# Kernel tuning notes

Hardware: AMD Instinct MI355X
Metric: run time of the kernel (lower is better)

The kernel has to match this reference:

```python
import jax, jax.numpy as jnp
import numpy as np

H = 400          # hidden_layers
D_CUR = 3 + 2 + 50   # X_CUR + X_WIN + X_ET
D_AC = 3 + 49        # X_AC + X_T
D_AP = 6 + 49        # X_AP + X_T


def _cell(x, h1, c1, h2, c2, Wx, U, b):
    """2-child child-sum LSTM cell (inferred CustomLSTMCell).
    x: [T, in]; h*/c*: [T, H]; Wx: [in, 4H]; U: [H, 4H]; b: [4H].
    Gate order: i, f, o, u. f uses a per-child recurrent term.
    """
    g = x @ Wx + b                            # [T, 4H]
    gi, gf, go, gu = jnp.split(g, 4, axis=-1)
    Ui, Uf, Uo, Uu = jnp.split(U, 4, axis=-1)
    hs = h1 + h2
    i = jax.nn.sigmoid(gi + hs @ Ui)
    f1 = jax.nn.sigmoid(gf + h1 @ Uf)
    f2 = jax.nn.sigmoid(gf + h2 @ Uf)
    o = jax.nn.sigmoid(go + hs @ Uo)
    u = jnp.tanh(gu + hs @ Uu)
    c = i * u + f1 * c1 + f2 * c2
    return o * jnp.tanh(c), c


def setup_inputs() -> dict:
    key = jax.random.key(0)
    T, IN = 8192, 55
    ks = iter(jax.random.split(key, 40))

    def p(*shape):
        return jax.random.normal(next(ks), shape, dtype=jnp.float32) * 0.05

    inp = {
        "x_temp": jax.random.normal(next(ks), (T, IN), dtype=jnp.float32),
        "x_air": jax.random.normal(next(ks), (T, IN), dtype=jnp.float32),
    }
    for name, d_in in [("t1", IN), ("t2", H), ("t3", H), ("a1", IN), ("a2", H), ("a3", H)]:
        inp[f"Wx_{name}"] = p(d_in, 4 * H)
        inp[f"U_{name}"] = p(H, 4 * H)
        inp[f"b_{name}"] = p(4 * H)
    inp["W_cur"] = p(2 * H, D_CUR); inp["b_cur"] = p(D_CUR)
    inp["W_ac"] = p(H, D_AC);       inp["b_ac"] = p(D_AC)
    inp["W_ap"] = p(H, D_AP);       inp["b_ap"] = p(D_AP)
    return inp


def reference(x_temp, x_air,
              Wx_t1, U_t1, b_t1, Wx_t2, U_t2, b_t2, Wx_t3, U_t3, b_t3,
              Wx_a1, U_a1, b_a1, Wx_a2, U_a2, b_a2, Wx_a3, U_a3, b_a3,
              W_cur, b_cur, W_ac, b_ac, W_ap, b_ap):
    T = x_temp.shape[0]
    z = jnp.zeros((T, H), dtype=x_temp.dtype)
    # States are re-zeroed every timestep in the original loop, so all
    # timesteps are independent and we batch them along axis 0.
    ht, ct = _cell(x_temp, z, z, z, z, Wx_t1, U_t1, b_t1)
    ha, ca = _cell(x_air,  z, z, z, z, Wx_a1, U_a1, b_a1)
    ht2, ct2 = _cell(ht, ht, ct, ha, ca, Wx_t2, U_t2, b_t2)
    ha2, ca2 = _cell(ha, ht, ct, ha, ca, Wx_a2, U_a2, b_a2)
    ht3, _ = _cell(ht2, ht2, ct2, ha2, ca2, Wx_t3, U_t3, b_t3)
    ha3, _ = _cell(ha2, ht2, ct2, ha2, ca2, Wx_a3, U_a3, b_a3)
    out_cur_win_t = jnp.concatenate([ht3, ha3], axis=-1) @ W_cur + b_cur  # [T, 55]
    out_ac_tet = ht3 @ W_ac + b_ac                                        # [T, 52]
    out_ap_aet = ha3 @ W_ap + b_ap                                        # [T, 55]
    return out_cur_win_t, out_ac_tet, out_ap_aet
```

## Files before the change

### kernel.cpp

```cpp
#include <hip/hip_runtime.h>
#include <hip/hip_bf16.h>

typedef unsigned short u16;
typedef unsigned int u32;
typedef unsigned long long u64;
typedef __attribute__((ext_vector_type(4))) float f32x4;
typedef __attribute__((ext_vector_type(8))) short s16x8;

__device__ inline u16 f2bf(float f) {
  union { float f; u32 u; } v; v.f = f;
  u32 r = (v.u + 0x7FFFu + ((v.u >> 16) & 1u)) >> 16;
  return (u16)r;
}
__device__ inline float bf2f(u16 h) { return __uint_as_float((u32)h << 16); }
__device__ inline float sigf(float x) { return 1.0f / (1.0f + __expf(-x)); }
__device__ inline float tanhf_(float x) {
  float ax = fabsf(x);
  float e = __expf(-2.0f * ax);
  float r = (1.0f - e) / (1.0f + e);
  return copysignf(r, x);
}
__device__ inline f32x4 ld4bf(const u16* p) {
  u64 v = *(const u64*)p;
  f32x4 r;
  r.x = __uint_as_float((u32)(v & 0xFFFFu) << 16);
  r.y = __uint_as_float((u32)((v >> 16) & 0xFFFFu) << 16);
  r.z = __uint_as_float((u32)((v >> 32) & 0xFFFFu) << 16);
  r.w = __uint_as_float((u32)((v >> 48) & 0xFFFFu) << 16);
  return r;
}
__device__ inline void gload16(const u16* g, u16* l) {
  __builtin_amdgcn_global_load_lds(
      (const __attribute__((address_space(1))) void*)(g),
      (__attribute__((address_space(3))) void*)(l), 16, 0, 0);
}

#define GLD 4096

__global__ void zero_pads(u16* __restrict__ A1, u16* __restrict__ A2,
                          u16* __restrict__ A3) {
  int idx = blockIdx.x * 256 + threadIdx.x;
  if (idx >= 196608) return;
  int b = idx / 65536, r = idx % 65536;
  int t = r / 8, q = r % 8;
  u16* A = (b == 0) ? A1 : (b == 1) ? A2 : A3;
  *(u64*)(A + (size_t)t * 832 + 800 + q * 4) = 0ULL;
}

__global__ void pad_cast(const float* __restrict__ src, u16* __restrict__ dst,
                         int srcCols, int dstCols, int rows) {
  int idx = blockIdx.x * 256 + threadIdx.x;
  if (idx >= rows * dstCols) return;
  int r = idx / dstCols, c = idx % dstCols;
  float v = (c < srcCols) ? src[r * srcCols + c] : 0.f;
  dst[idx] = f2bf(v);
}

__global__ void transpose_cast(const float* __restrict__ src, u16* __restrict__ dst,
                               int srcK, int srcN) {
  int idx = blockIdx.x * 256 + threadIdx.x;
  if (idx >= 64 * 1664) return;
  int k = idx / 1664, n = idx % 1664;
  float v = (k < srcK && n < srcN) ? src[k * srcN + n] : 0.f;
  dst[n * 64 + k] = f2bf(v);
}

__global__ void build_cell_B(const float* __restrict__ WxT, const float* __restrict__ UT,
                             const float* __restrict__ WxA, const float* __restrict__ UA,
                             u16* __restrict__ dst) {
  int idx = blockIdx.x * 256 + threadIdx.x;
  if (idx >= 4096 * 832) return;
  int r = idx / 4096, np = idx % 4096;
  int cell = np >> 11;
  int n = np & 2047;
  float v = 0.f;
  if (n < 2000 && r < 800) {
    int g = n / 400, j = n % 400;
    bool htside = (r < 400);
    int rr = htside ? r : r - 400;
    const float* Wx = cell ? WxA : WxT;
    const float* U  = cell ? UA  : UT;
    int gc = (g == 0) ? j : (g <= 2) ? 400 + j : (g == 3) ? 800 + j : 1200 + j;
    float wx = Wx[rr * 1600 + gc];
    float uu = U [rr * 1600 + gc];
    if (cell == 0) {
      if (htside) v = (g == 2) ? wx : wx + uu;
      else        v = (g == 1) ? 0.f : uu;
    } else {
      if (htside) v = (g == 2) ? 0.f : uu;
      else        v = (g == 1) ? wx : wx + uu;
    }
  }
  dst[(size_t)np * 832 + r] = f2bf(v);
}

__global__ void build_proj_B(const float* __restrict__ Wcur, const float* __restrict__ Wac,
                             const float* __restrict__ Wap, u16* __restrict__ dst) {
  int idx = blockIdx.x * 256 + threadIdx.x;
  if (idx >= 256 * 832) return;
  int n = idx / 832, r = idx % 832;
  float v = 0.f;
  if (r < 800) {
    if (n < 55) v = Wcur[r * 55 + n];
    else if (n < 107) { if (r < 400) v = Wac[r * 52 + (n - 55)]; }
    else if (n < 162) { if (r >= 400) v = Wap[(r - 400) * 55 + (n - 107)]; }
  }
  dst[idx] = f2bf(v);
}

__global__ __launch_bounds__(256) void gemm_lds(
    const u16* __restrict__ A, const u16* __restrict__ Bt,
    u16* __restrict__ C, int K, int ldc) {
  __shared__ u16 As[128 * 64];
  __shared__ u16 Bs[128 * 64];
  const int tid = threadIdx.x;
  const int lane = tid & 63;
  const int wid = tid >> 6;

  const int nwg = gridDim.x * gridDim.y;
  const int bid = blockIdx.y * gridDim.x + blockIdx.x;
  const int swz = (bid & 7) * (nwg >> 3) + (bid >> 3);
  const int m0 = (swz / gridDim.x) * 128;
  const int n0 = (swz % gridDim.x) * 128;

  const int wm = (wid >> 1) << 6;
  const int wn = (wid & 1) << 6;

  f32x4 acc[4][4];
#pragma unroll
  for (int i = 0; i < 4; ++i)
#pragma unroll
    for (int j = 0; j < 4; ++j) acc[i][j] = (f32x4){0.f, 0.f, 0.f, 0.f};

  const int nkt = K >> 6;
  const int l8 = lane >> 3, lb = lane & 7;
  const int scol = (lb ^ l8) << 3;
  const u16* gA = A + (size_t)(m0 + wid * 8 + l8) * K + scol;
  const u16* gB = Bt + (size_t)(n0 + wid * 8 + l8) * K + scol;
  u16* lA = As + wid * 8 * 64;
  u16* lB = Bs + wid * 8 * 64;

  const int kq = (lane >> 4) << 3;
  const int rrow = lane & 15;

  for (int kt = 0; kt < nkt; ++kt) {
    __syncthreads();
    const u16* pa = gA + kt * 64;
    const u16* pb = gB + kt * 64;
#pragma unroll
    for (int c = 0; c < 4; ++c) {
      gload16(pa + (size_t)(c * 32) * K, lA + c * 2048);
      gload16(pb + (size_t)(c * 32) * K, lB + c * 2048);
    }
    __syncthreads();
#pragma unroll
    for (int half = 0; half < 2; ++half) {
      const int kk = half * 32 + kq;
      s16x8 af[4], bfr[4];
#pragma unroll
      for (int f = 0; f < 4; ++f) {
        int ar = wm + f * 16 + rrow;
        af[f] = *(const s16x8*)((const char*)As + ar * 128 + ((kk * 2) ^ ((ar & 7) << 4)));
        int br = wn + f * 16 + rrow;
        bfr[f] = *(const s16x8*)((const char*)Bs + br * 128 + ((kk * 2) ^ ((br & 7) << 4)));
      }
#pragma unroll
      for (int i = 0; i < 4; ++i)
#pragma unroll
        for (int j = 0; j < 4; ++j)
          acc[i][j] = __builtin_amdgcn_mfma_f32_16x16x32_bf16(af[i], bfr[j], acc[i][j], 0, 0, 0);
    }
  }

  const int crow0 = m0 + wm + ((lane >> 4) << 2);
  const int ccol0 = n0 + wn + rrow;
#pragma unroll
  for (int i = 0; i < 4; ++i)
#pragma unroll
    for (int j = 0; j < 4; ++j)
#pragma unroll
      for (int r = 0; r < 4; ++r)
        C[(size_t)(crow0 + i * 16 + r) * ldc + (ccol0 + j * 16)] = f2bf(acc[i][j][r]);
}

__global__ void ep1(const u16* __restrict__ G,
                    const float* __restrict__ bT, const float* __restrict__ bA,
                    u16* __restrict__ Aout,
                    float* __restrict__ CT, float* __restrict__ CA) {
  int idx = blockIdx.x * 256 + threadIdx.x;
  if (idx >= 8192 * 200) return;
  int t = idx / 200, r = idx % 200;
  int cell = r / 100, j0 = (r % 100) * 4;
  const u16* g = G + (size_t)t * GLD + cell * 2048;
  const float* b = cell ? bA : bT;
  float* Cout = cell ? CA : CT;
  f32x4 ip = ld4bf(g + j0);
  f32x4 op = ld4bf(g + 800 + j0);
  f32x4 up = ld4bf(g + 1200 + j0);
  u64 hv = 0;
  f32x4 cv;
#pragma unroll
  for (int k = 0; k < 4; ++k) {
    int j = j0 + k;
    float c = sigf(ip[k] + b[j]) * tanhf_(up[k] + b[1200 + j]);
    float h = sigf(op[k] + b[800 + j]) * tanhf_(c);
    cv[k] = c;
    hv |= (u64)f2bf(h) << (16 * k);
  }
  *(u64*)(Aout + (size_t)t * 832 + cell * 400 + j0) = hv;
  *(f32x4*)(Cout + (size_t)t * 400 + j0) = cv;
}

__global__ void ep2(const u16* __restrict__ G,
                    const float* __restrict__ bT, const float* __restrict__ bA,
                    const float* __restrict__ C1, const float* __restrict__ C2,
                    u16* __restrict__ Aout,
                    float* __restrict__ CT, float* __restrict__ CA) {
  int idx = blockIdx.x * 256 + threadIdx.x;
  if (idx >= 8192 * 200) return;
  int t = idx / 200, r = idx % 200;
  int cell = r / 100, j0 = (r % 100) * 4;
  const u16* g = G + (size_t)t * GLD + cell * 2048;
  const float* b = cell ? bA : bT;
  float* Cout = cell ? CA : CT;
  f32x4 ip  = ld4bf(g + j0);
  f32x4 f1p = ld4bf(g + 400 + j0);
  f32x4 f2p = ld4bf(g + 800 + j0);
  f32x4 op  = ld4bf(g + 1200 + j0);
  f32x4 up  = ld4bf(g + 1600 + j0);
  f32x4 c1 = *(const f32x4*)(C1 + (size_t)t * 400 + j0);
  f32x4 c2 = *(const f32x4*)(C2 + (size_t)t * 400 + j0);
  u64 hv = 0;
  f32x4 cv;
#pragma unroll
  for (int k = 0; k < 4; ++k) {
    int j = j0 + k;
    float c = sigf(ip[k] + b[j]) * tanhf_(up[k] + b[1200 + j])
            + sigf(f1p[k] + b[400 + j]) * c1[k]
            + sigf(f2p[k] + b[400 + j]) * c2[k];
    float h = sigf(op[k] + b[800 + j]) * tanhf_(c);
    cv[k] = c;
    hv |= (u64)f2bf(h) << (16 * k);
  }
  *(u64*)(Aout + (size_t)t * 832 + cell * 400 + j0) = hv;
  if (Cout) *(f32x4*)(Cout + (size_t)t * 400 + j0) = cv;
}

__global__ void ep_out(const u16* __restrict__ G,
                       const float* __restrict__ bcur, const float* __restrict__ bac,
                       const float* __restrict__ bap, float* __restrict__ out) {
  int idx = blockIdx.x * 256 + threadIdx.x;
  if (idx >= 8192 * 162) return;
  int t = idx / 162, j = idx % 162;
  float v = bf2f(G[(size_t)t * GLD + j]);
  if (j < 55)       out[t * 55 + j] = v + bcur[j];
  else if (j < 107) out[450560 + t * 52 + (j - 55)] = v + bac[j - 55];
  else              out[876544 + t * 55 + (j - 107)] = v + bap[j - 107];
}

extern "C" void kernel_launch(void* const* d_in, const int* in_sizes, int n_in,
                              void* d_out, int out_size, void* d_ws, size_t ws_size,
                              hipStream_t stream) {
  const float* x_temp = (const float*)d_in[0];
  const float* x_air  = (const float*)d_in[1];
  const float* Wx_t1  = (const float*)d_in[2];
  const float* b_t1   = (const float*)d_in[4];
  const float* Wx_t2  = (const float*)d_in[5];
  const float* U_t2   = (const float*)d_in[6];
  const float* b_t2   = (const float*)d_in[7];
  const float* Wx_t3  = (const float*)d_in[8];
  const float* U_t3   = (const float*)d_in[9];
  const float* b_t3   = (const float*)d_in[10];
  const float* Wx_a1  = (const float*)d_in[11];
  const float* b_a1   = (const float*)d_in[13];
  const float* Wx_a2  = (const float*)d_in[14];
  const float* U_a2   = (const float*)d_in[15];
  const float* b_a2   = (const float*)d_in[16];
  const float* Wx_a3  = (const float*)d_in[17];
  const float* U_a3   = (const float*)d_in[18];
  const float* b_a3   = (const float*)d_in[19];
  const float* W_cur  = (const float*)d_in[20];
  const float* b_cur  = (const float*)d_in[21];
  const float* W_ac   = (const float*)d_in[22];
  const float* b_ac   = (const float*)d_in[23];
  const float* W_ap   = (const float*)d_in[24];
  const float* b_ap   = (const float*)d_in[25];

  char* ws = (char*)d_ws;
  u16*   A0t = (u16*)(ws + 0);
  u16*   A0a = (u16*)(ws + 1048576);
  u16*   B1t = (u16*)(ws + 2097152);
  u16*   B1a = (u16*)(ws + 2310144);
  u16*   Bp  = (u16*)(ws + 2523136);
  u16*   A1  = (u16*)(ws + 2949120);
  u16*   A2  = (u16*)(ws + 16580608);
  u16*   A3  = (u16*)(ws + 30212096);
  float* Ct  = (float*)(ws + 43843584);
  float* Ca  = (float*)(ws + 56950784);
  float* C2t = (float*)(ws + 70057984);
  float* C2a = (float*)(ws + 83165184);
  u16*   B2  = (u16*)(ws + 96272384);
  u16*   B3  = (u16*)(ws + 103088128);
  u16*   G   = (u16*)(ws + 109903872);
  float* out = (float*)d_out;

  dim3 blk(256);
  zero_pads<<<768, blk, 0, stream>>>(A1, A2, A3);
  pad_cast<<<2048, blk, 0, stream>>>(x_temp, A0t, 55, 64, 8192);
  pad_cast<<<2048, blk, 0, stream>>>(x_air,  A0a, 55, 64, 8192);
  transpose_cast<<<416, blk, 0, stream>>>(Wx_t1, B1t, 55, 1600);
  transpose_cast<<<416, blk, 0, stream>>>(Wx_a1, B1a, 55, 1600);
  build_cell_B<<<13312, blk, 0, stream>>>(Wx_t2, U_t2, Wx_a2, U_a2, B2);
  build_cell_B<<<13312, blk, 0, stream>>>(Wx_t3, U_t3, Wx_a3, U_a3, B3);
  build_proj_B<<<832, blk, 0, stream>>>(W_cur, W_ac, W_ap, Bp);

  gemm_lds<<<dim3(13, 64), blk, 0, stream>>>(A0t, B1t, G, 64, GLD);
  gemm_lds<<<dim3(13, 64), blk, 0, stream>>>(A0a, B1a, G + 2048, 64, GLD);
  ep1<<<6400, blk, 0, stream>>>(G, b_t1, b_a1, A1, Ct, Ca);
  gemm_lds<<<dim3(32, 64), blk, 0, stream>>>(A1, B2, G, 832, GLD);
  ep2<<<6400, blk, 0, stream>>>(G, b_t2, b_a2, Ct, Ca, A2, C2t, C2a);
  gemm_lds<<<dim3(32, 64), blk, 0, stream>>>(A2, B3, G, 832, GLD);
  ep2<<<6400, blk, 0, stream>>>(G, b_t3, b_a3, C2t, C2a, A3, nullptr, nullptr);
  gemm_lds<<<dim3(2, 64), blk, 0, stream>>>(A3, Bp, G, 832, GLD);
  ep_out<<<5184, blk, 0, stream>>>(G, b_cur, b_ac, b_ap, out);
}
```

Baseline: 417.7 us.

## Add triple-buffered pipelined GEMM for layer-2/3 cells and tile-transpose weight build

Adds a new 512-thread GEMM kernel for the two large 8192x4096x832 cell GEMMs. It uses 256x128 tiles, a triple-buffered LDS pipeline fed by async global-to-LDS loads with explicit vmcnt waits, an XOR-swizzled LDS layout and workgroup-ID swizzling. This is meant to hide global load latency and avoid bank conflicts. The weight-building kernel is also rewritten to go through a shared-memory tile transpose, so its global reads and writes are coalesced instead of strided. The new GEMM uses 144KB of LDS and hardcoded sizes, which limits occupancy and flexibility.

```diff
diff --git a/kernel.cpp b/kernel.cpp
--- a/kernel.cpp
+++ b/kernel.cpp
@@ -65,33 +65,50 @@
   dst[n * 64 + k] = f2bf(v);
 }
 
-__global__ void build_cell_B(const float* __restrict__ WxT, const float* __restrict__ UT,
-                             const float* __restrict__ WxA, const float* __restrict__ UA,
-                             u16* __restrict__ dst) {
-  int idx = blockIdx.x * 256 + threadIdx.x;
-  if (idx >= 4096 * 832) return;
-  int r = idx / 4096, np = idx % 4096;
-  int cell = np >> 11;
-  int n = np & 2047;
-  float v = 0.f;
-  if (n < 2000 && r < 800) {
-    int g = n / 400, j = n % 400;
-    bool htside = (r < 400);
-    int rr = htside ? r : r - 400;
-    const float* Wx = cell ? WxA : WxT;
-    const float* U  = cell ? UA  : UT;
-    int gc = (g == 0) ? j : (g <= 2) ? 400 + j : (g == 3) ? 800 + j : 1200 + j;
-    float wx = Wx[rr * 1600 + gc];
-    float uu = U [rr * 1600 + gc];
-    if (cell == 0) {
-      if (htside) v = (g == 2) ? wx : wx + uu;
-      else        v = (g == 1) ? 0.f : uu;
-    } else {
-      if (htside) v = (g == 2) ? 0.f : uu;
-      else        v = (g == 1) ? wx : wx + uu;
-    }
-  }
-  dst[(size_t)np * 832 + r] = f2bf(v);
+__global__ __launch_bounds__(256) void build_cell_B(
+    const float* __restrict__ WxT, const float* __restrict__ UT,
+    const float* __restrict__ WxA, const float* __restrict__ UA,
+    u16* __restrict__ dst) {
+  __shared__ float tile[64][65];
+  const int np0 = blockIdx.x * 64;
+  const int r0 = blockIdx.y * 64;
+  const int tx = threadIdx.x & 63, ty = threadIdx.x >> 6;
+
+  const int np = np0 + tx;
+  const int cell = np >> 11;
+  const int n = np & 2047;
+  const float* Wx = cell ? WxA : WxT;
+  const float* U  = cell ? UA  : UT;
+  int g = 0, j = 0, gc = 0;
+  if (n < 2000) {
+    g = n / 400; j = n % 400;
+    gc = (g == 0) ? j : (g <= 2) ? 400 + j : (g == 3) ? 800 + j : 1200 + j;
+  }
+#pragma unroll
+  for (int it = 0; it < 16; ++it) {
+    int r = r0 + it * 4 + ty;
+    float v = 0.f;
+    if (n < 2000 && r < 800) {
+      bool htside = (r < 400);
+      int rr = htside ? r : r - 400;
+      float wx = Wx[rr * 1600 + gc];
+      float uu = U [rr * 1600 + gc];
+      if (cell == 0) {
+        if (htside) v = (g == 2) ? wx : wx + uu;
+        else        v = (g == 1) ? 0.f : uu;
+      } else {
+        if (htside) v = (g == 2) ? 0.f : uu;
+        else        v = (g == 1) ? wx : wx + uu;
+      }
+    }
+    tile[tx][it * 4 + ty] = v;
+  }
+  __syncthreads();
+#pragma unroll
+  for (int it = 0; it < 16; ++it) {
+    int npw = np0 + it * 4 + ty;
+    dst[(size_t)npw * 832 + r0 + tx] = f2bf(tile[it * 4 + ty][tx]);
+  }
 }
 
 __global__ void build_proj_B(const float* __restrict__ Wcur, const float* __restrict__ Wac,
@@ -181,6 +198,123 @@
 #pragma unroll
       for (int r = 0; r < 4; ++r)
         C[(size_t)(crow0 + i * 16 + r) * ldc + (ccol0 + j * 16)] = f2bf(acc[i][j][r]);
+}
+
+#define PK 832
+#define PNKT 13
+#define ABY 32768
+#define BBY 16384
+#define BUFB 49152
+
+__global__ __launch_bounds__(512, 2) void gemm_pipe(
+    const u16* __restrict__ A, const u16* __restrict__ Bt,
+    u16* __restrict__ C, int ldc) {
+  __shared__ char sm[3 * BUFB];
+  const int tid = threadIdx.x;
+  const int lane = tid & 63;
+  const int wid = tid >> 6;
+
+  const int nwg = gridDim.x * gridDim.y;
+  const int bid = blockIdx.y * gridDim.x + blockIdx.x;
+  const int swz = (bid & 7) * (nwg >> 3) + (bid >> 3);
+  const int m0 = (swz / gridDim.x) * 256;
+  const int n0 = (swz % gridDim.x) * 128;
+
+  const int wr = wid >> 1;
+  const int wc = wid & 1;
+
+  f32x4 acc[4][4];
+#pragma unroll
+  for (int i = 0; i < 4; ++i)
+#pragma unroll
+    for (int j = 0; j < 4; ++j) acc[i][j] = (f32x4){0.f, 0.f, 0.f, 0.f};
+
+  const int q = lane >> 3, lb = lane & 7;
+  const int scol = (lb ^ q) << 3;
+  const u16* gA = A + (size_t)(m0 + wid * 8 + q) * PK + scol;
+  const u16* gB = Bt + (size_t)(n0 + wid * 8 + q) * PK + scol;
+  const int wrow = wid * 8;
+
+  const int kq = (lane >> 4) << 3;
+  const int rrow = lane & 15;
+
+#define STAGE(kt, buf)                                                        \
+  {                                                                           \
+    char* bb = sm + (buf) * BUFB;                                             \
+    const u16* pa = gA + (kt) * 64;                                           \
+    const u16* pb = gB + (kt) * 64;                                           \
+    gload16(pa,                  (u16*)(bb + (0 * 64 + wrow) * 128));         \
+    gload16(pa + 64 * PK,        (u16*)(bb + (1 * 64 + wrow) * 128));         \
+    gload16(pa + 128 * PK,       (u16*)(bb + (2 * 64 + wrow) * 128));         \
+    gload16(pa + 192 * PK,       (u16*)(bb + (3 * 64 + wrow) * 128));         \
+    gload16(pb,                  (u16*)(bb + ABY + (0 * 64 + wrow) * 128));   \
+    gload16(pb + 64 * PK,        (u16*)(bb + ABY + (1 * 64 + wrow) * 128));   \
+  }
+
+  STAGE(0, 0);
+  STAGE(1, 1);
+
+  int cbuf = 0;
+  int sbuf = 2;
+  for (int k = 0; k < PNKT; ++k) {
+    __builtin_amdgcn_sched_barrier(0);
+    __builtin_amdgcn_s_barrier();
+    if (k < PNKT - 2) {
+      STAGE(k + 2, sbuf);
+      asm volatile("s_waitcnt vmcnt(12)" ::: "memory");
+    } else if (k == PNKT - 2) {
+      asm volatile("s_waitcnt vmcnt(6)" ::: "memory");
+    } else {
+      asm volatile("s_waitcnt vmcnt(0)" ::: "memory");
+    }
+    __builtin_amdgcn_s_barrier();
+    __builtin_amdgcn_sched_barrier(0);
+
+    const char* bb = sm + cbuf * BUFB;
+    s16x8 af[4][2], bfr[4][2];
+#pragma unroll
+    for (int i = 0; i < 4; ++i) {
+      int ar = wr * 64 + i * 16 + rrow;
+      const char* base = bb + ar * 128;
+#pragma unroll
+      for (int h = 0; h < 2; ++h) {
+        int kk2 = (h * 32 + kq) * 2;
+        af[i][h] = *(const s16x8*)(base + (kk2 ^ ((ar & 7) << 4)));
+      }
+    }
+#pragma unroll
+    for (int jf = 0; jf < 4; ++jf) {
+      int br = wc * 64 + jf * 16 + rrow;
+      const char* base = bb + ABY + br * 128;
+#pragma unroll
+      for (int h = 0; h < 2; ++h) {
+        int kk2 = (h * 32 + kq) * 2;
+        bfr[jf][h] = *(const s16x8*)(base + (kk2 ^ ((br & 7) << 4)));
+      }
+    }
+#pragma unroll
+    for (int i = 0; i < 4; ++i)
+#pragma unroll
+      for (int jf = 0; jf < 4; ++jf)
+#pragma unroll
+        for (int h = 0; h < 2; ++h)
+          acc[i][jf] = __builtin_amdgcn_mfma_f32_16x16x32_bf16(
+              af[i][h], bfr[jf][h], acc[i][jf], 0, 0, 0);
+
+    cbuf = (cbuf == 2) ? 0 : cbuf + 1;
+    sbuf = (sbuf == 2) ? 0 : sbuf + 1;
+  }
+#undef STAGE
+
+  const int crow0 = m0 + wr * 64 + ((lane >> 4) << 2);
+  const int ccol0 = n0 + wc * 64 + rrow;
+#pragma unroll
+  for (int i = 0; i < 4; ++i)
+#pragma unroll
+    for (int jf = 0; jf < 4; ++jf)
+#pragma unroll
+      for (int r = 0; r < 4; ++r)
+        C[(size_t)(crow0 + i * 16 + r) * ldc + (ccol0 + jf * 16)] = f2bf(acc[i][jf][r]);
 }
 
 __global__ void ep1(const u16* __restrict__ G,
@@ -310,16 +444,16 @@
   pad_cast<<<2048, blk, 0, stream>>>(x_air,  A0a, 55, 64, 8192);
   transpose_cast<<<416, blk, 0, stream>>>(Wx_t1, B1t, 55, 1600);
   transpose_cast<<<416, blk, 0, stream>>>(Wx_a1, B1a, 55, 1600);
-  build_cell_B<<<13312, blk, 0, stream>>>(Wx_t2, U_t2, Wx_a2, U_a2, B2);
-  build_cell_B<<<13312, blk, 0, stream>>>(Wx_t3, U_t3, Wx_a3, U_a3, B3);
+  build_cell_B<<<dim3(64, 13), blk, 0, stream>>>(Wx_t2, U_t2, Wx_a2, U_a2, B2);
+  build_cell_B<<<dim3(64, 13), blk, 0, stream>>>(Wx_t3, U_t3, Wx_a3, U_a3, B3);
   build_proj_B<<<832, blk, 0, stream>>>(W_cur, W_ac, W_ap, Bp);
 
   gemm_lds<<<dim3(13, 64), blk, 0, stream>>>(A0t, B1t, G, 64, GLD);
   gemm_lds<<<dim3(13, 64), blk, 0, stream>>>(A0a, B1a, G + 2048, 64, GLD);
   ep1<<<6400, blk, 0, stream>>>(G, b_t1, b_a1, A1, Ct, Ca);
-  gemm_lds<<<dim3(32, 64), blk, 0, stream>>>(A1, B2, G, 832, GLD);
+  gemm_pipe<<<dim3(32, 32), dim3(512), 0, stream>>>(A1, B2, G, GLD);
   ep2<<<6400, blk, 0, stream>>>(G, b_t2, b_a2, Ct, Ca, A2, C2t, C2a);
-  gemm_lds<<<dim3(32, 64), blk, 0, stream>>>(A2, B3, G, 832, GLD);
+  gemm_pipe<<<dim3(32, 32), dim3(512), 0, stream>>>(A2, B3, G, GLD);
   ep2<<<6400, blk, 0, stream>>>(G, b_t3, b_a3, C2t, C2a, A3, nullptr, nullptr);
   gemm_lds<<<dim3(2, 64), blk, 0, stream>>>(A3, Bp, G, 832, GLD);
   ep_out<<<5184, blk, 0, stream>>>(G, b_cur, b_ac, b_ap, out);
```

Result: faster. 407.2 us (-2.5%).

## Add 256x256 8-wave pipelined GEMM for hidden cells, tile weight build

Applied to the files above, without the earlier changes.

Adds a new 512-thread GEMM kernel with 256x256 output tiles, double-buffered swizzled LDS, staged global loads interleaved with MFMA quarters, priority hints and an LDS-staged coalesced epilogue, used for the two large 8192x4096x832 cell GEMMs. It also rewrites the weight-building kernel to transpose through shared memory so both reads and writes are coalesced. The ep2 epilogue now handles both cells per thread so each thread loads c1/c2 once. The larger tiles raise data reuse and cut global traffic, at the cost of heavy LDS use (128KB) and fewer resident blocks.

```diff
diff --git a/kernel.cpp b/kernel.cpp
--- a/kernel.cpp
+++ b/kernel.cpp
@@ -6,6 +6,7 @@
 typedef unsigned long long u64;
 typedef __attribute__((ext_vector_type(4))) float f32x4;
 typedef __attribute__((ext_vector_type(8))) short s16x8;
+typedef __attribute__((ext_vector_type(4))) int i32x4;
 
 __device__ inline u16 f2bf(float f) {
   union { float f; u32 u; } v; v.f = f;
@@ -65,33 +66,50 @@
   dst[n * 64 + k] = f2bf(v);
 }
 
-__global__ void build_cell_B(const float* __restrict__ WxT, const float* __restrict__ UT,
-                             const float* __restrict__ WxA, const float* __restrict__ UA,
-                             u16* __restrict__ dst) {
-  int idx = blockIdx.x * 256 + threadIdx.x;
-  if (idx >= 4096 * 832) return;
-  int r = idx / 4096, np = idx % 4096;
-  int cell = np >> 11;
-  int n = np & 2047;
-  float v = 0.f;
-  if (n < 2000 && r < 800) {
-    int g = n / 400, j = n % 400;
-    bool htside = (r < 400);
-    int rr = htside ? r : r - 400;
-    const float* Wx = cell ? WxA : WxT;
-    const float* U  = cell ? UA  : UT;
-    int gc = (g == 0) ? j : (g <= 2) ? 400 + j : (g == 3) ? 800 + j : 1200 + j;
-    float wx = Wx[rr * 1600 + gc];
-    float uu = U [rr * 1600 + gc];
-    if (cell == 0) {
-      if (htside) v = (g == 2) ? wx : wx + uu;
-      else        v = (g == 1) ? 0.f : uu;
-    } else {
-      if (htside) v = (g == 2) ? 0.f : uu;
-      else        v = (g == 1) ? wx : wx + uu;
-    }
-  }
-  dst[(size_t)np * 832 + r] = f2bf(v);
+__global__ __launch_bounds__(256) void build_cell_B(
+    const float* __restrict__ WxT, const float* __restrict__ UT,
+    const float* __restrict__ WxA, const float* __restrict__ UA,
+    u16* __restrict__ dst) {
+  __shared__ float tile[64][65];
+  const int np0 = blockIdx.x * 64;
+  const int r0 = blockIdx.y * 64;
+  const int tx = threadIdx.x & 63, ty = threadIdx.x >> 6;
+
+  const int np = np0 + tx;
+  const int cell = np >> 11;
+  const int n = np & 2047;
+  const float* Wx = cell ? WxA : WxT;
+  const float* U  = cell ? UA  : UT;
+  int g = 0, j = 0, gc = 0;
+  if (n < 2000) {
+    g = n / 400; j = n % 400;
+    gc = (g == 0) ? j : (g <= 2) ? 400 + j : (g == 3) ? 800 + j : 1200 + j;
+  }
+#pragma unroll
+  for (int it = 0; it < 16; ++it) {
+    int r = r0 + it * 4 + ty;
+    float v = 0.f;
+    if (n < 2000 && r < 800) {
+      bool htside = (r < 400);
+      int rr = htside ? r : r - 400;
+      float wx = Wx[rr * 1600 + gc];
+      float uu = U [rr * 1600 + gc];
+      if (cell == 0) {
+        if (htside) v = (g == 2) ? wx : wx + uu;
+        else        v = (g == 1) ? 0.f : uu;
+      } else {
+        if (htside) v = (g == 2) ? 0.f : uu;
+        else        v = (g == 1) ? wx : wx + uu;
+      }
+    }
+    tile[tx][it * 4 + ty] = v;
+  }
+  __syncthreads();
+#pragma unroll
+  for (int it = 0; it < 16; ++it) {
+    int npw = np0 + it * 4 + ty;
+    dst[(size_t)npw * 832 + r0 + tx] = f2bf(tile[it * 4 + ty][tx]);
+  }
 }
 
 __global__ void build_proj_B(const float* __restrict__ Wcur, const float* __restrict__ Wac,
@@ -181,6 +199,183 @@
 #pragma unroll
       for (int r = 0; r < 4; ++r)
         C[(size_t)(crow0 + i * 16 + r) * ldc + (ccol0 + j * 16)] = f2bf(acc[i][j][r]);
+}
+
+#define PK8 832
+#define NT8 13
+
+__global__ __launch_bounds__(512, 2) void gemm_8p(
+    const u16* __restrict__ A, const u16* __restrict__ Bt,
+    u16* __restrict__ C, int ldc) {
+  __shared__ char sm[131072];
+  const int tid = threadIdx.x;
+  const int lane = tid & 63;
+  const int wid = tid >> 6;
+
+  const int nwg = gridDim.x * gridDim.y;
+  const int bid = blockIdx.y * gridDim.x + blockIdx.x;
+  const int swz = (bid & 7) * (nwg >> 3) + (bid >> 3);
+  const int m0 = (swz / gridDim.x) * 256;
+  const int n0 = (swz % gridDim.x) * 256;
+
+  const int wr = wid >> 2;
+  const int wc = wid & 3;
+
+  f32x4 acc[8][4];
+#pragma unroll
+  for (int i = 0; i < 8; ++i)
+#pragma unroll
+    for (int j = 0; j < 4; ++j) acc[i][j] = (f32x4){0.f, 0.f, 0.f, 0.f};
+
+  const int rr8 = tid >> 3;
+  const int scol = ((tid & 7) ^ (rr8 & 7)) << 3;
+  const u16* gA = A + (size_t)(m0 + rr8) * PK8 + scol;
+  const u16* gB = Bt + (size_t)(n0 + rr8) * PK8 + scol;
+  const int ldso = wid << 10;
+
+#define SA8(kt, buf, c) gload16(gA + (size_t)((c) * 64) * PK8 + (kt) * 64,   \
+      (u16*)(sm + (buf) * 65536 + (c) * 8192 + ldso))
+#define SB8(kt, buf, c) gload16(gB + (size_t)((c) * 64) * PK8 + (kt) * 64,   \
+      (u16*)(sm + (buf) * 65536 + 32768 + (c) * 8192 + ldso))
+#define FENCE_BAR { __builtin_amdgcn_sched_barrier(0); __builtin_amdgcn_s_barrier(); __builtin_amdgcn_sched_barrier(0); }
+
+  const int kq = (lane >> 4) << 3;
+  const int rrow = lane & 15;
+
+  SA8(0, 0, 0); SA8(0, 0, 2);
+  SB8(0, 0, 0); SB8(0, 0, 1); SB8(0, 0, 2); SB8(0, 0, 3);
+  SA8(0, 0, 1); SA8(0, 0, 3);
+
+  for (int t = 0; t < NT8; ++t) {
+    const char* bb = sm + (t & 1) * 65536;
+    const int nb = (t & 1) ^ 1;
+    const bool st = (t + 1 < NT8);
+    s16x8 afr[4][2], bfr[2][2];
+
+    if (st) { SA8(t + 1, nb, 0); SA8(t + 1, nb, 2);
+              asm volatile("s_waitcnt vmcnt(4)" ::: "memory"); }
+    else    { asm volatile("s_waitcnt vmcnt(2)" ::: "memory"); }
+    FENCE_BAR;
+#pragma unroll
+    for (int mf = 0; mf < 4; ++mf) {
+      int ar = wr * 128 + mf * 16 + rrow;
+      const char* ab = bb + ar * 128;
+#pragma unroll
+      for (int kh = 0; kh < 2; ++kh)
+        afr[mf][kh] = *(const s16x8*)(ab + (((kh * 32 + kq) * 2) ^ ((ar & 7) << 4)));
+    }
+#pragma unroll
+    for (int nf = 0; nf < 2; ++nf) {
+      int br = wc * 64 + nf * 16 + rrow;
+      const char* bbp = bb + 32768 + br * 128;
+#pragma unroll
+      for (int kh = 0; kh < 2; ++kh)
+        bfr[nf][kh] = *(const s16x8*)(bbp + (((kh * 32 + kq) * 2) ^ ((br & 7) << 4)));
+    }
+    __builtin_amdgcn_s_setprio(1);
+#pragma unroll
+    for (int mf = 0; mf < 4; ++mf)
+#pragma unroll
+      for (int nf = 0; nf < 2; ++nf)
+#pragma unroll
+        for (int kh = 0; kh < 2; ++kh)
+          acc[mf][nf] = __builtin_amdgcn_mfma_f32_16x16x32_bf16(
+              afr[mf][kh], bfr[nf][kh], acc[mf][nf], 0, 0, 0);
+    __builtin_amdgcn_s_setprio(0);
+    FENCE_BAR;
+
+    if (st) { SB8(t + 1, nb, 0); SB8(t + 1, nb, 1);
+              asm volatile("s_waitcnt vmcnt(4)" ::: "memory"); }
+    else    { asm volatile("s_waitcnt vmcnt(0)" ::: "memory"); }
+    FENCE_BAR;
+#pragma unroll
+    for (int nf = 0; nf < 2; ++nf) {
+      int br = wc * 64 + 32 + nf * 16 + rrow;
+      const char* bbp = bb + 32768 + br * 128;
+#pragma unroll
+      for (int kh = 0; kh < 2; ++kh)
+        bfr[nf][kh] = *(const s16x8*)(bbp + (((kh * 32 + kq) * 2) ^ ((br & 7) << 4)));
+    }
+    __builtin_amdgcn_s_setprio(1);
+#pragma unroll
+    for (int mf = 0; mf < 4; ++mf)
+#pragma unroll
+      for (int nf = 0; nf < 2; ++nf)
+#pragma unroll
+        for (int kh = 0; kh < 2; ++kh)
+          acc[mf][2 + nf] = __builtin_amdgcn_mfma_f32_16x16x32_bf16(
+              afr[mf][kh], bfr[nf][kh], acc[mf][2 + nf], 0, 0, 0);
+    __builtin_amdgcn_s_setprio(0);
+    FENCE_BAR;
+
+    if (st) { SB8(t + 1, nb, 2); SB8(t + 1, nb, 3); }
+    FENCE_BAR;
+#pragma unroll
+    for (int mf = 0; mf < 4; ++mf) {
+      int ar = wr * 128 + 64 + mf * 16 + rrow;
+      const char* ab = bb + ar * 128;
+#pragma unroll
+      for (int kh = 0; kh < 2; ++kh)
+        afr[mf][kh] = *(const s16x8*)(ab + (((kh * 32 + kq) * 2) ^ ((ar & 7) << 4)));
+    }
+    __builtin_amdgcn_s_setprio(1);
+#pragma unroll
+    for (int mf = 0; mf < 4; ++mf)
+#pragma unroll
+      for (int nf = 0; nf < 2; ++nf)
+#pragma unroll
+        for (int kh = 0; kh < 2; ++kh)
+          acc[4 + mf][2 + nf] = __builtin_amdgcn_mfma_f32_16x16x32_bf16(
+              afr[mf][kh], bfr[nf][kh], acc[4 + mf][2 + nf], 0, 0, 0);
+    __builtin_amdgcn_s_setprio(0);
+    FENCE_BAR;
+
+    if (st) { SA8(t + 1, nb, 1); SA8(t + 1, nb, 3); }
+    FENCE_BAR;
+#pragma unroll
+    for (int nf = 0; nf < 2; ++nf) {
+      int br = wc * 64 + nf * 16 + rrow;
+      const char* bbp = bb + 32768 + br * 128;
+#pragma unroll
+      for (int kh = 0; kh < 2; ++kh)
+        bfr[nf][kh] = *(const s16x8*)(bbp + (((kh * 32 + kq) * 2) ^ ((br & 7) << 4)));
+    }
+    __builtin_amdgcn_s_setprio(1);
+#pragma unroll
+    for (int mf = 0; mf < 4; ++mf)
+#pragma unroll
+      for (int nf = 0; nf < 2; ++nf)
+#pragma unroll
+        for (int kh = 0; kh < 2; ++kh)
+          acc[4 + mf][nf] = __builtin_amdgcn_mfma_f32_16x16x32_bf16(
+              afr[mf][kh], bfr[nf][kh], acc[4 + mf][nf], 0, 0, 0);
+    __builtin_amdgcn_s_setprio(0);
+    FENCE_BAR;
+  }
+#undef SA8
+#undef SB8
+#undef FENCE_BAR
+
+  u16* eps = (u16*)(sm + wid * 16384);
+#pragma unroll
+  for (int i = 0; i < 8; ++i)
+#pragma unroll
+    for (int j = 0; j < 4; ++j)
+#pragma unroll
+      for (int r = 0; r < 4; ++r) {
+        int row = i * 16 + ((lane >> 4) << 2) + r;
+        int colb = (j * 16 + rrow) * 2;
+        *(u16*)((char*)eps + row * 128 + (colb ^ ((row & 7) << 4))) = f2bf(acc[i][j][r]);
+      }
+  const size_t crowW = m0 + wr * 128;
+  const int ccolW = n0 + wc * 64;
+#pragma unroll
+  for (int p = 0; p < 16; ++p) {
+    int row = p * 8 + (lane >> 3);
+    int segb = (lane & 7) * 16;
+    i32x4 v = *(const i32x4*)((char*)eps + row * 128 + (segb ^ ((row & 7) << 4)));
+    *(i32x4*)(C + (crowW + row) * (size_t)ldc + ccolW + (lane & 7) * 8) = v;
+  }
 }
 
 __global__ void ep1(const u16* __restrict__ G,
@@ -217,33 +412,37 @@
                     u16* __restrict__ Aout,
                     float* __restrict__ CT, float* __restrict__ CA) {
   int idx = blockIdx.x * 256 + threadIdx.x;
-  if (idx >= 8192 * 200) return;
-  int t = idx / 200, r = idx % 200;
-  int cell = r / 100, j0 = (r % 100) * 4;
-  const u16* g = G + (size_t)t * GLD + cell * 2048;
-  const float* b = cell ? bA : bT;
-  float* Cout = cell ? CA : CT;
-  f32x4 ip  = ld4bf(g + j0);
-  f32x4 f1p = ld4bf(g + 400 + j0);
-  f32x4 f2p = ld4bf(g + 800 + j0);
-  f32x4 op  = ld4bf(g + 1200 + j0);
-  f32x4 up  = ld4bf(g + 1600 + j0);
+  if (idx >= 8192 * 100) return;
+  int t = idx / 100, j0 = (idx % 100) * 4;
   f32x4 c1 = *(const f32x4*)(C1 + (size_t)t * 400 + j0);
   f32x4 c2 = *(const f32x4*)(C2 + (size_t)t * 400 + j0);
-  u64 hv = 0;
-  f32x4 cv;
-#pragma unroll
-  for (int k = 0; k < 4; ++k) {
-    int j = j0 + k;
-    float c = sigf(ip[k] + b[j]) * tanhf_(up[k] + b[1200 + j])
-            + sigf(f1p[k] + b[400 + j]) * c1[k]
-            + sigf(f2p[k] + b[400 + j]) * c2[k];
-    float h = sigf(op[k] + b[800 + j]) * tanhf_(c);
-    cv[k] = c;
-    hv |= (u64)f2bf(h) << (16 * k);
-  }
-  *(u64*)(Aout + (size_t)t * 832 + cell * 400 + j0) = hv;
-  if (Cout) *(f32x4*)(Cout + (size_t)t * 400 + j0) = cv;
+#pragma unroll
+  for (int cell = 0; cell < 2; ++cell) {
+    const u16* g = G + (size_t)t * GLD + cell * 2048;
+    const float* b = cell ? bA : bT;
+    f32x4 ip  = ld4bf(g + j0);
+    f32x4 f1p = ld4bf(g + 400 + j0);
+    f32x4 f2p = ld4bf(g + 800 + j0);
+    f32x4 op  = ld4bf(g + 1200 + j0);
+    f32x4 up  = ld4bf(g + 1600 + j0);
+    u64 hv = 0;
+    f32x4 cv;
+#pragma unroll
+    for (int k = 0; k < 4; ++k) {
+      int j = j0 + k;
+      float c = sigf(ip[k] + b[j]) * tanhf_(up[k] + b[1200 + j])
+              + sigf(f1p[k] + b[400 + j]) * c1[k]
+              + sigf(f2p[k] + b[400 + j]) * c2[k];
+      float h = sigf(op[k] + b[800 + j]) * tanhf_(c);
+      cv[k] = c;
+      hv |= (u64)f2bf(h) << (16 * k);
+    }
+    *(u64*)(Aout + (size_t)t * 832 + cell * 400 + j0) = hv;
+    if (CT) {
+      float* Cout = cell ? CA : CT;
+      *(f32x4*)(Cout + (size_t)t * 400 + j0) = cv;
+    }
+  }
 }
 
 __global__ void ep_out(const u16* __restrict__ G,
@@ -310,17 +509,17 @@
   pad_cast<<<2048, blk, 0, stream>>>(x_air,  A0a, 55, 64, 8192);
   transpose_cast<<<416, blk, 0, stream>>>(Wx_t1, B1t, 55, 1600);
   transpose_cast<<<416, blk, 0, stream>>>(Wx_a1, B1a, 55, 1600);
-  build_cell_B<<<13312, blk, 0, stream>>>(Wx_t2, U_t2, Wx_a2, U_a2, B2);
-  build_cell_B<<<13312, blk, 0, stream>>>(Wx_t3, U_t3, Wx_a3, U_a3, B3);
+  build_cell_B<<<dim3(64, 13), blk, 0, stream>>>(Wx_t2, U_t2, Wx_a2, U_a2, B2);
+  build_cell_B<<<dim3(64, 13), blk, 0, stream>>>(Wx_t3, U_t3, Wx_a3, U_a3, B3);
   build_proj_B<<<832, blk, 0, stream>>>(W_cur, W_ac, W_ap, Bp);
 
   gemm_lds<<<dim3(13, 64), blk, 0, stream>>>(A0t, B1t, G, 64, GLD);
   gemm_lds<<<dim3(13, 64), blk, 0, stream>>>(A0a, B1a, G + 2048, 64, GLD);
   ep1<<<6400, blk, 0, stream>>>(G, b_t1, b_a1, A1, Ct, Ca);
-  gemm_lds<<<dim3(32, 64), blk, 0, stream>>>(A1, B2, G, 832, GLD);
-  ep2<<<6400, blk, 0, stream>>>(G, b_t2, b_a2, Ct, Ca, A2, C2t, C2a);
-  gemm_lds<<<dim3(32, 64), blk, 0, stream>>>(A2, B3, G, 832, GLD);
-  ep2<<<6400, blk, 0, stream>>>(G, b_t3, b_a3, C2t, C2a, A3, nullptr, nullptr);
+  gemm_8p<<<dim3(16, 32), dim3(512), 0, stream>>>(A1, B2, G, GLD);
+  ep2<<<3200, blk, 0, stream>>>(G, b_t2, b_a2, Ct, Ca, A2, C2t, C2a);
+  gemm_8p<<<dim3(16, 32), dim3(512), 0, stream>>>(A2, B3, G, GLD);
+  ep2<<<3200, blk, 0, stream>>>(G, b_t3, b_a3, C2t, C2a, A3, nullptr, nullptr);
   gemm_lds<<<dim3(2, 64), blk, 0, stream>>>(A3, Bp, G, 832, GLD);
   ep_out<<<5184, blk, 0, stream>>>(G, b_cur, b_ac, b_ap, out);
 }
```

After: 373.8 us. 1.12x faster.
